# Performance work log

Hardware: AMD Instinct MI355X
Metric: run time of the kernel (lower is better)

Reference implementation:

```python
import jax, jax.numpy as jnp
import numpy as np

B, F_DIM, C, M = 16, 64, 64, 512
OUT_CH = 32
DT = 1.0


def setup_inputs() -> dict:
    key = jax.random.key(0)
    ks = jax.random.split(key, 8)
    x = jax.random.normal(ks[0], (B, F_DIM, C, M), dtype=jnp.float32)
    A = jax.random.uniform(ks[1], (B, M, C, C), dtype=jnp.float32)
    phys_prior = jax.random.normal(ks[2], (B, C, M), dtype=jnp.float32)
    kappa = jnp.array(0.1, dtype=jnp.float32)
    alpha = jnp.array(0.05, dtype=jnp.float32)
    # r_phi MLP: Linear(1,16) -> ELU -> Linear(16,1)
    w1 = jax.random.normal(ks[3], (16, 1), dtype=jnp.float32) * 1.0
    b1 = jnp.zeros((16,), dtype=jnp.float32)
    w2 = jax.random.normal(ks[4], (1, 16), dtype=jnp.float32) * 0.25
    b2 = jnp.zeros((1,), dtype=jnp.float32)
    # 1x1 Conv2d(1, OUT_CH): weight (OUT_CH,1,1,1) -> flatten to (OUT_CH,)
    pw = jax.random.normal(ks[5], (OUT_CH,), dtype=jnp.float32)
    pb = jnp.zeros((OUT_CH,), dtype=jnp.float32)
    return {"x": x, "A": A, "phys_prior": phys_prior, "kappa": kappa,
            "alpha": alpha, "w1": w1, "b1": b1, "w2": w2, "b2": b2,
            "pw": pw, "pb": pb}


def reference(x, A, phys_prior, kappa, alpha, w1, b1, w2, b2, pw, pb):
    # x: (B,F,C,M), A: (B,M,C,C), phys_prior: (B,C,M)
    s = x.mean(axis=1)                      # (B,C,M)
    deg = A.sum(axis=-1)                    # (B,M,C)
    sT = jnp.transpose(s, (0, 2, 1))        # (B,M,C)
    # torch einsum 'bmcd,bmcn->bmdn' with n=1 contracts over c: (A^T s)
    As = jnp.einsum('bmcd,bmc->bmd', A, sT)  # (B,M,C)
    Ls = jnp.transpose(deg * sT - As, (0, 2, 1))  # (B,C,M)
    k = jax.nn.softplus(kappa)
    # tiny MLP on per-(b,c) mean over M
    r_in = s.mean(axis=-1, keepdims=True)   # (B,C,1)
    h = jax.nn.elu(r_in @ w1.T + b1)        # (B,C,16)
    r = h @ w2.T + b2                       # (B,C,1), broadcasts over M
    phys_corr = alpha * phys_prior          # (B,C,M)
    s_new = s - DT * k * Ls + DT * (r + phys_corr)  # (B,C,M)
    # 1x1 conv over (B,1,C,M): pointwise scale+bias per output channel
    corr = s_new[:, None, :, :] * pw[None, :, None, None] + pb[None, :, None, None]
    return corr  # (B,OUT_CH,C,M)
```

## Files before the change

kernel.cpp:

```cpp
#include <hip/hip_runtime.h>
#include <math.h>

#define B_  16
#define F_  64
#define C_  64
#define M_  512
#define OC_ 32

typedef float vf4 __attribute__((ext_vector_type(4)));

__global__ __launch_bounds__(128, 6) void k1_mean(
    const float* __restrict__ x,
    float* __restrict__ s_out, float* __restrict__ rpart)
{
    const int gid = blockIdx.x;
    const int q   = gid & 3;
    const int bc  = gid >> 2;
    const int b   = bc >> 6;
    const int c   = bc & 63;
    const int t   = threadIdx.x;
    const int tf  = t >> 5;
    const int tm  = t & 31;
    const int m4  = (q << 5) + tm;

    const size_t rowbase = ((size_t)b * F_ * C_ + c) * M_;
    float ax = 0.f, ay = 0.f, az = 0.f, aw = 0.f;
    #pragma unroll 8
    for (int j = 0; j < 16; ++j) {
        const int f = (tf << 4) + j;
        const float4 v = ((const float4*)(x + rowbase + (size_t)f * C_ * M_))[m4];
        ax += v.x; ay += v.y; az += v.z; aw += v.w;
    }

    __shared__ float4 red[4][32];
    red[tf][tm] = make_float4(ax, ay, az, aw);
    __syncthreads();

    if (tf == 0) {
        const float4 r1 = red[1][tm], r2 = red[2][tm], r3 = red[3][tm];
        const float inv_f = 1.0f / (float)F_;
        float4 sv;
        sv.x = (ax + r1.x + r2.x + r3.x) * inv_f;
        sv.y = (ay + r1.y + r2.y + r3.y) * inv_f;
        sv.z = (az + r1.z + r2.z + r3.z) * inv_f;
        sv.w = (aw + r1.w + r2.w + r3.w) * inv_f;
        ((float4*)(s_out + (size_t)bc * M_))[m4] = sv;

        float p = sv.x + sv.y + sv.z + sv.w;
        #pragma unroll
        for (int off = 16; off > 0; off >>= 1) p += __shfl_xor(p, off);
        if (t == 0) rpart[gid] = p;
    }
}

__global__ __launch_bounds__(1024, 8) void k2_fused(
    const float* __restrict__ A, const float* __restrict__ phys,
    const float* __restrict__ kappa_p, const float* __restrict__ alpha_p,
    const float* __restrict__ s_in, const float* __restrict__ rpart,
    const float* __restrict__ w1, const float* __restrict__ b1,
    const float* __restrict__ w2, const float* __restrict__ b2,
    const float* __restrict__ pw, const float* __restrict__ pb,
    float* __restrict__ out)
{
    __shared__ float Ab[2][4096];
    __shared__ float sl[16 * 68];
    __shared__ float ph[16 * 68];
    __shared__ float snl[64 * 17];
    __shared__ float redA[16 * 64];
    __shared__ float degL[2][C_];

    const int t   = threadIdx.x;
    const int blk = blockIdx.x;
    const int b   = blk >> 5;
    const int m0  = (blk & 31) << 4;

    {
        const int cc = t >> 4;
        const int mi = t & 15;
        const size_t gg = ((size_t)(b * C_ + cc)) * M_ + m0 + mi;
        sl[mi * 68 + cc] = s_in[gg];
        ph[mi * 68 + cc] = phys[gg];
    }

    float r_c = 0.f;
    if (t < 64) {
        const float4 rp = ((const float4*)rpart)[b * C_ + t];
        const float rin = (rp.x + rp.y + rp.z + rp.w) * (1.0f / (float)M_);
        r_c = b2[0];
        #pragma unroll
        for (int j = 0; j < 16; ++j) {
            float hh = rin * w1[j] + b1[j];
            hh = (hh > 0.f) ? hh : (expf(hh) - 1.f);
            r_c += hh * w2[j];
        }
    }

    const float* Abase = A + (size_t)(b * M_ + m0) * (C_ * C_);
    const int h    = t & 15;
    const int rowi = t >> 4;
    const int c    = t & 63;
    const int g    = t >> 6;

    auto stage_and_deg = [&](const float4& vv, int buf) {
        ((float4*)Ab[buf])[t] = vv;
        float p = vv.x + vv.y + vv.z + vv.w;
        p += __shfl_xor(p, 1);
        p += __shfl_xor(p, 2);
        p += __shfl_xor(p, 4);
        p += __shfl_xor(p, 8);
        if (h == 0) degL[buf][rowi] = p;
    };

    auto compute = [&](int buf, int i) {
        const float s0 = sl[i * 68 + 4 * g + 0];
        const float s1 = sl[i * 68 + 4 * g + 1];
        const float s2 = sl[i * 68 + 4 * g + 2];
        const float s3 = sl[i * 68 + 4 * g + 3];
        const float ap = Ab[buf][(4 * g + 0) * 64 + c] * s0
                       + Ab[buf][(4 * g + 1) * 64 + c] * s1
                       + Ab[buf][(4 * g + 2) * 64 + c] * s2
                       + Ab[buf][(4 * g + 3) * 64 + c] * s3;
        redA[g * 64 + c] = ap;
    };

    const float kcoef = log1pf(expf(kappa_p[0]));
    const float al    = alpha_p[0];

    auto combine = [&](int buf, int i) {
        if (t < 64) {
            float As = 0.f;
            #pragma unroll
            for (int q2 = 0; q2 < 16; ++q2) As += redA[q2 * 64 + t];
            const float dg   = degL[buf][t];
            const float sval = sl[i * 68 + t];
            const float pv   = ph[i * 68 + t];
            snl[t * 17 + i] = sval - kcoef * (dg * sval - As) + (r_c + al * pv);
        }
    };

    float4 vA = ((const float4*)Abase)[t];
    stage_and_deg(vA, 0);
    float4 vB = ((const float4*)(Abase + 4096))[t];
    __syncthreads();

    #pragma unroll 1
    for (int ii = 0; ii < 8; ++ii) {
        const int i0 = 2 * ii;
        if (i0 + 2 < 16)
            vA = ((const float4*)(Abase + (size_t)(i0 + 2) * 4096))[t];
        compute(0, i0);
        stage_and_deg(vB, 1);
        __syncthreads();
        combine(0, i0);
        __syncthreads();

        const int i1 = i0 + 1;
        if (i1 + 2 < 16)
            vB = ((const float4*)(Abase + (size_t)(i1 + 2) * 4096))[t];
        compute(1, i1);
        if (i1 + 1 < 16)
            stage_and_deg(vA, 0);
        __syncthreads();
        combine(1, i1);
        __syncthreads();
    }

    #pragma unroll
    for (int i = 0; i < 8; ++i) {
        const int idx = (i << 10) + t;
        const int mq  = idx & 3;
        const int cc  = (idx >> 2) & 63;
        const int o   = idx >> 8;
        const float w  = pw[o];
        const float bb = pb[o];
        vf4 ov;
        ov.x = snl[cc * 17 + mq * 4 + 0] * w + bb;
        ov.y = snl[cc * 17 + mq * 4 + 1] * w + bb;
        ov.z = snl[cc * 17 + mq * 4 + 2] * w + bb;
        ov.w = snl[cc * 17 + mq * 4 + 3] * w + bb;
        __builtin_nontemporal_store(ov,
            (vf4*)(out + (((size_t)(b * OC_ + o)) * C_ + cc) * M_ + m0 + mq * 4));
    }
}

extern "C" void kernel_launch(void* const* d_in, const int* in_sizes, int n_in,
                              void* d_out, int out_size, void* d_ws, size_t ws_size,
                              hipStream_t stream)
{
    const float* x     = (const float*)d_in[0];
    const float* A     = (const float*)d_in[1];
    const float* phys  = (const float*)d_in[2];
    const float* kappa = (const float*)d_in[3];
    const float* alpha = (const float*)d_in[4];
    const float* w1    = (const float*)d_in[5];
    const float* b1    = (const float*)d_in[6];
    const float* w2    = (const float*)d_in[7];
    const float* b2    = (const float*)d_in[8];
    const float* pw    = (const float*)d_in[9];
    const float* pb    = (const float*)d_in[10];
    float* out = (float*)d_out;

    float* ws    = (float*)d_ws;
    float* s     = ws;
    float* rpart = ws + (size_t)B_ * C_ * M_;

    k1_mean<<<B_ * C_ * 4, 128, 0, stream>>>(x, s, rpart);
    k2_fused<<<B_ * (M_ / 16), 1024, 0, stream>>>(A, phys, kappa, alpha, s, rpart,
                                                  w1, b1, w2, b2, pw, pb, out);
}
```

Before: 65.47 us.

## Halve k2 block size to 512 threads with 8 m-slices and single-buffered A

Reworks the fused Laplacian kernel to use 512-thread blocks, each handling 8 m positions instead of 16, which doubles the grid to 1024 blocks. Each thread now loads two float4 of A per slice, and the LDS double buffer is replaced by a single buffer with register prefetch of the next slice. Each thread's partial dot product now covers 8 rows instead of 4. The aim is more blocks for better CU occupancy and load balance. The cost is an extra barrier per slice and less overlap between staging and compute.

```diff
diff --git a/kernel.cpp b/kernel.cpp
--- a/kernel.cpp
+++ b/kernel.cpp
@@ -53,7 +53,7 @@
     }
 }
 
-__global__ __launch_bounds__(1024, 8) void k2_fused(
+__global__ __launch_bounds__(512, 8) void k2_fused(
     const float* __restrict__ A, const float* __restrict__ phys,
     const float* __restrict__ kappa_p, const float* __restrict__ alpha_p,
     const float* __restrict__ s_in, const float* __restrict__ rpart,
@@ -62,21 +62,21 @@
     const float* __restrict__ pw, const float* __restrict__ pb,
     float* __restrict__ out)
 {
-    __shared__ float Ab[2][4096];
-    __shared__ float sl[16 * 68];
-    __shared__ float ph[16 * 68];
-    __shared__ float snl[64 * 17];
-    __shared__ float redA[16 * 64];
+    __shared__ float Ab[4096];
+    __shared__ float sl[8 * 68];
+    __shared__ float ph[8 * 68];
+    __shared__ float snl[64 * 9];
+    __shared__ float redA[8 * 64];
     __shared__ float degL[2][C_];
 
     const int t   = threadIdx.x;
     const int blk = blockIdx.x;
-    const int b   = blk >> 5;
-    const int m0  = (blk & 31) << 4;
+    const int b   = blk >> 6;
+    const int m0  = (blk & 63) << 3;
 
     {
-        const int cc = t >> 4;
-        const int mi = t & 15;
+        const int cc = t >> 3;
+        const int mi = t & 7;
         const size_t gg = ((size_t)(b * C_ + cc)) * M_ + m0 + mi;
         sl[mi * 68 + cc] = s_in[gg];
         ph[mi * 68 + cc] = phys[gg];
@@ -101,83 +101,70 @@
     const int c    = t & 63;
     const int g    = t >> 6;
 
-    auto stage_and_deg = [&](const float4& vv, int buf) {
-        ((float4*)Ab[buf])[t] = vv;
-        float p = vv.x + vv.y + vv.z + vv.w;
-        p += __shfl_xor(p, 1);
-        p += __shfl_xor(p, 2);
-        p += __shfl_xor(p, 4);
-        p += __shfl_xor(p, 8);
-        if (h == 0) degL[buf][rowi] = p;
-    };
-
-    auto compute = [&](int buf, int i) {
-        const float s0 = sl[i * 68 + 4 * g + 0];
-        const float s1 = sl[i * 68 + 4 * g + 1];
-        const float s2 = sl[i * 68 + 4 * g + 2];
-        const float s3 = sl[i * 68 + 4 * g + 3];
-        const float ap = Ab[buf][(4 * g + 0) * 64 + c] * s0
-                       + Ab[buf][(4 * g + 1) * 64 + c] * s1
-                       + Ab[buf][(4 * g + 2) * 64 + c] * s2
-                       + Ab[buf][(4 * g + 3) * 64 + c] * s3;
-        redA[g * 64 + c] = ap;
-    };
-
     const float kcoef = log1pf(expf(kappa_p[0]));
     const float al    = alpha_p[0];
 
-    auto combine = [&](int buf, int i) {
+    float4 vLo = ((const float4*)Abase)[t];
+    float4 vHi = ((const float4*)Abase)[t + 512];
+    __syncthreads();
+
+    #pragma unroll 1
+    for (int i = 0; i < 8; ++i) {
+        const int par = i & 1;
+
+        ((float4*)Ab)[t]       = vLo;
+        ((float4*)Ab)[t + 512] = vHi;
+
+        float p0 = vLo.x + vLo.y + vLo.z + vLo.w;
+        float p1 = vHi.x + vHi.y + vHi.z + vHi.w;
+        p0 += __shfl_xor(p0, 1); p1 += __shfl_xor(p1, 1);
+        p0 += __shfl_xor(p0, 2); p1 += __shfl_xor(p1, 2);
+        p0 += __shfl_xor(p0, 4); p1 += __shfl_xor(p1, 4);
+        p0 += __shfl_xor(p0, 8); p1 += __shfl_xor(p1, 8);
+        if (h == 0) {
+            degL[par][rowi]      = p0;
+            degL[par][rowi + 32] = p1;
+        }
+        __syncthreads();
+
+        if (i < 7) {
+            vLo = ((const float4*)(Abase + (size_t)(i + 1) * 4096))[t];
+            vHi = ((const float4*)(Abase + (size_t)(i + 1) * 4096))[t + 512];
+        }
+
+        const int j0 = g << 3;
+        float ap = 0.f;
+        #pragma unroll
+        for (int k = 0; k < 8; ++k)
+            ap += Ab[(j0 + k) * 64 + c] * sl[i * 68 + j0 + k];
+        redA[g * 64 + c] = ap;
+        __syncthreads();
+
         if (t < 64) {
             float As = 0.f;
             #pragma unroll
-            for (int q2 = 0; q2 < 16; ++q2) As += redA[q2 * 64 + t];
-            const float dg   = degL[buf][t];
+            for (int q2 = 0; q2 < 8; ++q2) As += redA[q2 * 64 + t];
+            const float dg   = degL[par][t];
             const float sval = sl[i * 68 + t];
             const float pv   = ph[i * 68 + t];
-            snl[t * 17 + i] = sval - kcoef * (dg * sval - As) + (r_c + al * pv);
+            snl[t * 9 + i] = sval - kcoef * (dg * sval - As) + (r_c + al * pv);
         }
-    };
-
-    float4 vA = ((const float4*)Abase)[t];
-    stage_and_deg(vA, 0);
-    float4 vB = ((const float4*)(Abase + 4096))[t];
+    }
     __syncthreads();
-
-    #pragma unroll 1
-    for (int ii = 0; ii < 8; ++ii) {
-        const int i0 = 2 * ii;
-        if (i0 + 2 < 16)
-            vA = ((const float4*)(Abase + (size_t)(i0 + 2) * 4096))[t];
-        compute(0, i0);
-        stage_and_deg(vB, 1);
-        __syncthreads();
-        combine(0, i0);
-        __syncthreads();
-
-        const int i1 = i0 + 1;
-        if (i1 + 2 < 16)
-            vB = ((const float4*)(Abase + (size_t)(i1 + 2) * 4096))[t];
-        compute(1, i1);
-        if (i1 + 1 < 16)
-            stage_and_deg(vA, 0);
-        __syncthreads();
-        combine(1, i1);
-        __syncthreads();
-    }
 
     #pragma unroll
     for (int i = 0; i < 8; ++i) {
-        const int idx = (i << 10) + t;
-        const int mq  = idx & 3;
-        const int cc  = (idx >> 2) & 63;
-        const int o   = idx >> 8;
+        const int idx = (i << 9) + t;
+        const int mq  = idx & 1;
+        const int cc  = (idx >> 1) & 63;
+        const int o   = idx >> 7;
         const float w  = pw[o];
         const float bb = pb[o];
         vf4 ov;
-        ov.x = snl[cc * 17 + mq * 4 + 0] * w + bb;
-        ov.y = snl[cc * 17 + mq * 4 + 1] * w + bb;
-        ov.z = snl[cc * 17 + mq * 4 + 2] * w + bb;
-        ov.w = snl[cc * 17 + mq * 4 + 3] * w + bb;
+        ov.x = snl[cc * 9 + mq * 4 + 0] * w + bb;
+        ov.y = snl[cc * 9 + mq * 4 + 1] * w + bb;
+        ov.z = snl[cc * 9 + mq * 4 + 2] * w + bb;
+        ov.w = snl[cc * 9 + mq * 4 + 3] * w + bb;
         __builtin_nontemporal_store(ov,
             (vf4*)(out + (((size_t)(b * OC_ + o)) * C_ + cc) * M_ + m0 + mq * 4));
     }
@@ -205,6 +192,6 @@
     float* rpart = ws + (size_t)B_ * C_ * M_;
 
     k1_mean<<<B_ * C_ * 4, 128, 0, stream>>>(x, s, rpart);
-    k2_fused<<<B_ * (M_ / 16), 1024, 0, stream>>>(A, phys, kappa, alpha, s, rpart,
-                                                  w1, b1, w2, b2, pw, pb, out);
+    k2_fused<<<B_ * (M_ / 8), 512, 0, stream>>>(A, phys, kappa, alpha, s, rpart,
+                                                w1, b1, w2, b2, pw, pb, out);
 }
```

Measured after the change: 120.2 us. +83.6%, slower.
